# Performance work log

Measured on AMD Instinct MI355X. Metric: run time of the kernel, lower is better.

Reference implementation:

```python
import jax, jax.numpy as jnp
import numpy as np

EPS = 1e-6  # rms_norm_eps
Q_EPS = 1e-5


def activation_quant(x):
    # per-token (last dim) absmax int8 quant
    scale = 127.0 / jnp.clip(jnp.max(jnp.abs(x), axis=-1, keepdims=True), Q_EPS, None)
    return jnp.clip(jnp.round(x * scale), -128, 127) / scale


def weight_quant(w):
    # ternary quant with global mean-absmax scale
    scale = 1.0 / jnp.clip(jnp.mean(jnp.abs(w)), Q_EPS, None)
    return jnp.clip(jnp.round(w * scale), -1, 1) / scale


def bit_linear(x, w):
    # straight-through estimator on both activation and weight quantization
    xq = x + jax.lax.stop_gradient(activation_quant(x) - x)
    wq = w + jax.lax.stop_gradient(weight_quant(w) - w)
    return jnp.einsum('...k,nk->...n', xq, wq)


def rmsnorm(x, w):
    var = jnp.mean(jnp.square(x), axis=-1, keepdims=True)
    return x * jax.lax.rsqrt(var + EPS) * w


def setup_inputs() -> dict:
    key = jax.random.key(0)
    ks = jax.random.split(key, 6)
    B, C, H, D, F, NC = 8, 3, 128, 2048, 8192, 1000
    return {
        'x': jax.random.normal(ks[0], (B, C, H, D), jnp.float32),
        'Wg': jax.random.normal(ks[1], (F, D), jnp.float32) * (D ** -0.5),
        'Wu': jax.random.normal(ks[2], (F, D), jnp.float32) * (D ** -0.5),
        'Wd': jax.random.normal(ks[3], (D, F), jnp.float32) * (F ** -0.5),
        'ln_w': jnp.ones((F,), jnp.float32),
        'cls_W': jax.random.normal(ks[4], (NC, C), jnp.float32) * (C ** -0.5),
        'cls_b': jnp.zeros((NC,), jnp.float32),
    }


def reference(x, Wg, Wu, Wd, ln_w, cls_W, cls_b):
    # BitNet SwiGLU MLP
    h = jax.nn.silu(bit_linear(x, Wg)) * bit_linear(x, Wu)  # [B,3,H,F]
    h = rmsnorm(h, ln_w)
    h = bit_linear(h, Wd)  # [B,3,H,D]
    # classifier: AdaptiveAvgPool2d((1,1)) over last two dims -> [B,3] -> Linear
    pooled = jnp.mean(h, axis=(2, 3))  # [B,3]
    return pooled @ cls_W.T + cls_b  # [B, num_classes]
```

## Files before the change

### kernel.cpp

```cpp
#include <hip/hip_runtime.h>
#include <stdint.h>

#define BB 8
#define CC 3
#define HH 128
#define DD 2048
#define FF 8192
#define NCLS 1000
#define MTOK (BB*CC*HH)
#define NW   (FF*DD)
#define INV_NW (1.0f/16777216.0f)

typedef __attribute__((ext_vector_type(4))) int i32x4;
typedef __attribute__((ext_vector_type(16))) int i32x16;
typedef _Float16 f16x8 __attribute__((ext_vector_type(8)));

#define WS_SUMS    0
#define WS_PART    256
#define WS_POOLED  4096
#define WS_TSUM    16384
#define WS_INVSA   49152
#define WS_XQ      61440
#define WS_WGQ     6352896
#define WS_WUQ     23130112
#define WS_H       39907328
#define WS_NEED    90238976

__device__ __forceinline__ float reduce256(float v, float* red, bool first) {
  for (int off = 32; off > 0; off >>= 1) v += __shfl_xor(v, off);
  if (!first) __syncthreads();
  if ((threadIdx.x & 63) == 0) red[threadIdx.x >> 6] = v;
  __syncthreads();
  return (red[0] + red[1]) + (red[2] + red[3]);
}

__global__ __launch_bounds__(256) void prep_kernel(
    const float* __restrict__ Wg, const float* __restrict__ Wu,
    const float* __restrict__ Wd, const float* __restrict__ x,
    float* __restrict__ part, int8_t* __restrict__ xq,
    float* __restrict__ inv_sa, float* __restrict__ tsum) {
  const int bx = blockIdx.x, t = threadIdx.x;
  if (bx < 768) {
    const int mat = bx >> 8;
    const float* w = (mat == 0) ? Wg : (mat == 1) ? Wu : Wd;
    const float4* w4 = (const float4*)w;
    const unsigned idx = (bx & 255) * 256 + t;
    float s0 = 0.f, s1 = 0.f, s2 = 0.f, s3 = 0.f;
#pragma unroll 4
    for (int it = 0; it < 64; it += 4) {
      float4 a = w4[idx + (size_t)(it + 0) * 65536];
      float4 b = w4[idx + (size_t)(it + 1) * 65536];
      float4 c = w4[idx + (size_t)(it + 2) * 65536];
      float4 d = w4[idx + (size_t)(it + 3) * 65536];
      s0 += fabsf(a.x) + fabsf(a.y) + fabsf(a.z) + fabsf(a.w);
      s1 += fabsf(b.x) + fabsf(b.y) + fabsf(b.z) + fabsf(b.w);
      s2 += fabsf(c.x) + fabsf(c.y) + fabsf(c.z) + fabsf(c.w);
      s3 += fabsf(d.x) + fabsf(d.y) + fabsf(d.z) + fabsf(d.w);
    }
    __shared__ float red[4];
    float total = reduce256((s0 + s1) + (s2 + s3), red, true);
    if (t == 0) part[bx] = total;
  } else if (bx < 3840) {
    const int tok = bx - 768;
    const float* row = x + (size_t)tok * DD;
    float4 v0 = *(const float4*)(row + t * 4);
    float4 v1 = *(const float4*)(row + 1024 + t * 4);
    float mx = fmaxf(fmaxf(fmaxf(fabsf(v0.x), fabsf(v0.y)), fmaxf(fabsf(v0.z), fabsf(v0.w))),
                     fmaxf(fmaxf(fabsf(v1.x), fabsf(v1.y)), fmaxf(fabsf(v1.z), fabsf(v1.w))));
    for (int off = 32; off > 0; off >>= 1) mx = fmaxf(mx, __shfl_xor(mx, off));
    __shared__ float wm[4];
    if ((t & 63) == 0) wm[t >> 6] = mx;
    __syncthreads();
    float m = fmaxf(fmaxf(wm[0], wm[1]), fmaxf(wm[2], wm[3]));
    float mclip = fmaxf(m, 1e-5f);
    float sa = 127.0f / mclip;
    if (t == 0) inv_sa[tok] = mclip * (1.0f / 127.0f);
    float qv[8] = {v0.x, v0.y, v0.z, v0.w, v1.x, v1.y, v1.z, v1.w};
    unsigned p0 = 0, p1 = 0;
#pragma unroll
    for (int j = 0; j < 4; ++j) {
      int qi = (int)fminf(fmaxf(rintf(qv[j] * sa), -128.f), 127.f);
      p0 |= ((unsigned)(qi & 0xff)) << (8 * j);
    }
#pragma unroll
    for (int j = 0; j < 4; ++j) {
      int qi = (int)fminf(fmaxf(rintf(qv[4 + j] * sa), -128.f), 127.f);
      p1 |= ((unsigned)(qi & 0xff)) << (8 * j);
    }
    *(unsigned*)(xq + (size_t)tok * DD + t * 4) = p0;
    *(unsigned*)(xq + (size_t)tok * DD + 1024 + t * 4) = p1;
  } else {
    float4 z = {0.f, 0.f, 0.f, 0.f};
#pragma unroll
    for (int j = 0; j < 8; ++j)
      *(float4*)(tsum + j * 1024 + t * 4) = z;
  }
}

__global__ __launch_bounds__(256) void wquant_kernel(
    const float* __restrict__ Wg, const float* __restrict__ Wu,
    const float* __restrict__ Wd, const float* __restrict__ part,
    float* __restrict__ sums, int8_t* __restrict__ wgq,
    int8_t* __restrict__ wuq, float* __restrict__ tsum) {
  const int bx = blockIdx.x, t = threadIdx.x;
  __shared__ float red[4];
  if (bx < 8192) {
    const int mat = bx >> 12;
    const float* w = mat ? Wu : Wg;
    int8_t* wq = mat ? wuq : wgq;
    const float total = reduce256(part[mat * 256 + t], red, true);
    const float scale = 1.0f / fmaxf(total * INV_NW, 1e-5f);
    const unsigned base = (bx & 4095) * 4096;
    float4 v[4];
#pragma unroll
    for (int j = 0; j < 4; ++j)
      v[j] = *(const float4*)(w + base + j * 1024 + t * 4);
#pragma unroll
    for (int j = 0; j < 4; ++j) {
      float vv[4] = {v[j].x, v[j].y, v[j].z, v[j].w};
      unsigned p = 0;
#pragma unroll
      for (int jj = 0; jj < 4; ++jj) {
        int qi = (int)fminf(fmaxf(rintf(vv[jj] * scale), -1.f), 1.f);
        p |= ((unsigned)(qi & 0xff)) << (8 * jj);
      }
      *(unsigned*)(wq + base + j * 1024 + t * 4) = p;
    }
  } else {
    const int idx = bx - 8192;
    const int slab = idx >> 5, colg = idx & 31;
    const float totalWd = reduce256(part[512 + t], red, true);
    const float scale = 1.0f / fmaxf(totalWd * INV_NW, 1e-5f);
    const int col = colg * 256 + t;
    const float* wp = Wd + (size_t)(slab * 256) * FF + col;
    float acc = 0.f;
#pragma unroll 8
    for (int d = 0; d < 256; ++d)
      acc += fminf(fmaxf(rintf(wp[(size_t)d * FF] * scale), -1.f), 1.f);
    atomicAdd(&tsum[col], acc);
    if (idx == 255) {
      const float tg = reduce256(part[t], red, false);
      const float tu = reduce256(part[256 + t], red, false);
      if (t == 0) { sums[0] = tg; sums[1] = tu; sums[2] = totalWd; }
    }
  }
}

__device__ __forceinline__ void gl_lds16(const void* g, void* l) {
  __builtin_amdgcn_global_load_lds((const __attribute__((address_space(1))) void*)g,
                                   (__attribute__((address_space(3))) void*)l, 16, 0, 0);
}

__global__ __launch_bounds__(256, 4) void gemm_gu_kernel(
    const int8_t* __restrict__ Aq,
    const int8_t* __restrict__ Bgq,
    const int8_t* __restrict__ Buq,
    const float* __restrict__ inv_sa,
    const float* __restrict__ sums,
    _Float16* __restrict__ Hbuf)
{
  __shared__ int8_t ldsA[128 * 128];
  __shared__ int8_t ldsG[64 * 128];
  __shared__ int8_t ldsU[64 * 128];

  const int t = threadIdx.x;
  const int wave = t >> 6, lane = t & 63;
  const int l32 = lane & 31, l5 = lane >> 5;
  const int m0 = blockIdx.x * 128;
  const int n0 = blockIdx.y * 64;
  const int wm = (wave >> 1) * 64, wn = (wave & 1) * 32;

  i32x16 accg[2], accu[2];
#pragma unroll
  for (int i = 0; i < 2; ++i)
#pragma unroll
    for (int r = 0; r < 16; ++r) { accg[i][r] = 0; accu[i][r] = 0; }

  const int srow = lane >> 3;
  const int sp = lane & 7;

  for (int k0 = 0; k0 < DD; k0 += 128) {
    __syncthreads();
#pragma unroll
    for (int j = 0; j < 4; ++j) {
      const int rl = wave * 32 + j * 8 + srow;
      const int cg = sp ^ (rl & 7);
      gl_lds16(Aq + (size_t)(m0 + rl) * DD + k0 + cg * 16,
               ldsA + (wave * 32 + j * 8) * 128);
    }
#pragma unroll
    for (int j = 0; j < 2; ++j) {
      const int rl = wave * 16 + j * 8 + srow;
      const int cg = sp ^ (rl & 7);
      gl_lds16(Bgq + (size_t)(n0 + rl) * DD + k0 + cg * 16,
               ldsG + (wave * 16 + j * 8) * 128);
      gl_lds16(Buq + (size_t)(n0 + rl) * DD + k0 + cg * 16,
               ldsU + (wave * 16 + j * 8) * 128);
    }
    __syncthreads();

#pragma unroll
    for (int ks = 0; ks < 4; ++ks) {
      i32x4 af[2], gfv, ufv;
#pragma unroll
      for (int mt = 0; mt < 2; ++mt) {
        const int row = wm + mt * 32 + l32;
        const int p = (ks * 2 + l5) ^ (row & 7);
        af[mt] = *(const i32x4*)(ldsA + row * 128 + p * 16);
      }
      {
        const int row = wn + l32;
        const int p = (ks * 2 + l5) ^ (row & 7);
        gfv = *(const i32x4*)(ldsG + row * 128 + p * 16);
        ufv = *(const i32x4*)(ldsU + row * 128 + p * 16);
      }
#pragma unroll
      for (int mt = 0; mt < 2; ++mt) {
        accg[mt] = __builtin_amdgcn_mfma_i32_32x32x32_i8(af[mt], gfv, accg[mt], 0, 0, 0);
        accu[mt] = __builtin_amdgcn_mfma_i32_32x32x32_i8(af[mt], ufv, accu[mt], 0, 0, 0);
      }
    }
  }

  const float meanWg = fmaxf(sums[0] * INV_NW, 1e-5f);
  const float meanWu = fmaxf(sums[1] * INV_NW, 1e-5f);
  const int coln = n0 + wn + l32;
#pragma unroll
  for (int mt = 0; mt < 2; ++mt) {
#pragma unroll
    for (int r = 0; r < 16; ++r) {
      const int row = m0 + wm + mt * 32 + (r & 3) + 8 * (r >> 2) + 4 * l5;
      const float isa = inv_sa[row];
      const float g = (float)accg[mt][r] * (isa * meanWg);
      const float u = (float)accu[mt][r] * (isa * meanWu);
      const float sv = g / (1.0f + expf(-g));
      Hbuf[(size_t)row * FF + coln] = (_Float16)(sv * u);
    }
  }
}

__global__ __launch_bounds__(256) void rms_quant_dot_kernel(
    const _Float16* __restrict__ H, const float* __restrict__ lnw,
    const float* __restrict__ tsum, float* __restrict__ pooled) {
  const int tok = blockIdx.x, t = threadIdx.x;
  const _Float16* row = H + (size_t)tok * FF;
  f16x8 hv[4];
  float4 lw[8];
  float ssq = 0.f, mx = 0.f;
#pragma unroll
  for (int i = 0; i < 4; ++i) {
    hv[i] = *(const f16x8*)(row + i * 2048 + t * 8);
    lw[2 * i] = *(const float4*)(lnw + i * 2048 + t * 8);
    lw[2 * i + 1] = *(const float4*)(lnw + i * 2048 + t * 8 + 4);
    const float* lwp = (const float*)&lw[2 * i];
#pragma unroll
    for (int j = 0; j < 8; ++j) {
      float h = (float)hv[i][j];
      ssq += h * h;
      mx = fmaxf(mx, fabsf(h * lwp[j]));
    }
  }
  for (int off = 32; off > 0; off >>= 1) {
    ssq += __shfl_xor(ssq, off);
    mx = fmaxf(mx, __shfl_xor(mx, off));
  }
  __shared__ float rs[4], rm[4], ra[4];
  const int wave = t >> 6, lane = t & 63;
  if (lane == 0) { rs[wave] = ssq; rm[wave] = mx; }
  __syncthreads();
  const float S = (rs[0] + rs[1]) + (rs[2] + rs[3]);
  const float M = fmaxf(fmaxf(rm[0], rm[1]), fmaxf(rm[2], rm[3]));
  const float r = rsqrtf(S * (1.0f / (float)FF) + 1e-6f);
  const float mc = fmaxf(M * r, 1e-5f);
  const float as2 = 127.0f / mc;
  float acc = 0.f;
#pragma unroll
  for (int i = 0; i < 4; ++i) {
    float4 t0 = *(const float4*)(tsum + i * 2048 + t * 8);
    float4 t1 = *(const float4*)(tsum + i * 2048 + t * 8 + 4);
    const float* lwp = (const float*)&lw[2 * i];
    const float* tp0 = (const float*)&t0;
    const float* tp1 = (const float*)&t1;
#pragma unroll
    for (int j = 0; j < 8; ++j) {
      float ts = (j < 4) ? tp0[j] : tp1[j - 4];
      float y = (float)hv[i][j] * lwp[j] * r;
      acc += fminf(fmaxf(rintf(y * as2), -128.f), 127.f) * ts;
    }
  }
  for (int off = 32; off > 0; off >>= 1) acc += __shfl_xor(acc, off);
  if (lane == 0) ra[wave] = acc;
  __syncthreads();
  if (t == 0)
    pooled[tok] = ((ra[0] + ra[1]) + (ra[2] + ra[3])) * (mc * (1.0f / 127.0f));
}

__global__ __launch_bounds__(256) void classifier_kernel(
    const float* __restrict__ pooled, const float* __restrict__ sums,
    const float* __restrict__ clsW, const float* __restrict__ clsb,
    float* __restrict__ out) {
  const int b = blockIdx.x, t = threadIdx.x;
  const float meanWd = fmaxf(sums[2] * INV_NW, 1e-5f);
  const float sc = meanWd * (1.0f / (float)(HH * DD));
  __shared__ float ps[3];
#pragma unroll
  for (int c = 0; c < 3; ++c) {
    float s = 0.f;
    if (t < 64) {
      const float* base = pooled + (b * 3 + c) * 128;
      s = base[t] + base[t + 64];
      for (int off = 32; off > 0; off >>= 1) s += __shfl_xor(s, off);
      if (t == 0) ps[c] = s * sc;
    }
    __syncthreads();
  }
  const float p0 = ps[0], p1 = ps[1], p2 = ps[2];
  for (int n = t; n < NCLS; n += 256)
    out[b * NCLS + n] = clsb[n] + p0 * clsW[n * 3 + 0] + p1 * clsW[n * 3 + 1] + p2 * clsW[n * 3 + 2];
}

extern "C" void kernel_launch(void* const* d_in, const int* in_sizes, int n_in,
                              void* d_out, int out_size, void* d_ws, size_t ws_size,
                              hipStream_t stream) {
  if (n_in < 7 || ws_size < (size_t)WS_NEED) return;
  const float* x = (const float*)d_in[0];
  const float* Wg = (const float*)d_in[1];
  const float* Wu = (const float*)d_in[2];
  const float* Wd = (const float*)d_in[3];
  const float* lnw = (const float*)d_in[4];
  const float* clsW = (const float*)d_in[5];
  const float* clsb = (const float*)d_in[6];
  float* out = (float*)d_out;
  char* ws = (char*)d_ws;
  float* sums = (float*)(ws + WS_SUMS);
  float* part = (float*)(ws + WS_PART);
  float* pooled = (float*)(ws + WS_POOLED);
  float* tsum = (float*)(ws + WS_TSUM);
  float* inv_sa = (float*)(ws + WS_INVSA);
  int8_t* xq = (int8_t*)(ws + WS_XQ);
  int8_t* wgq = (int8_t*)(ws + WS_WGQ);
  int8_t* wuq = (int8_t*)(ws + WS_WUQ);
  _Float16* hbuf = (_Float16*)(ws + WS_H);

  prep_kernel<<<3841, 256, 0, stream>>>(Wg, Wu, Wd, x, part, xq, inv_sa, tsum);
  wquant_kernel<<<8448, 256, 0, stream>>>(Wg, Wu, Wd, part, sums, wgq, wuq, tsum);
  gemm_gu_kernel<<<dim3(24, 128), 256, 0, stream>>>(xq, wgq, wuq, inv_sa, sums, hbuf);
  rms_quant_dot_kernel<<<MTOK, 256, 0, stream>>>(hbuf, lnw, tsum, pooled);
  classifier_kernel<<<BB, 256, 0, stream>>>(pooled, sums, clsW, clsb, out);
  (void)in_sizes; (void)out_size;
}
```

Baseline: 392.4 us.

## Switch gate/up GEMM to 16x16x64 int8 MFMA and rebalance prep/quant grids

The gate/up GEMM now uses 16x16x64 int8 MFMA tiles with a 4x2 accumulator grid per wave in place of 32x32x32 tiles, and lowers the occupancy hint from 4 to 3. The weight abs-sum prep is split into many more small contiguous blocks (6144 partials) and the weight quant kernel gives each block twice as many elements. The Wd column-sum slabs are halved. The aim is higher MFMA throughput, fewer LDS reads per FLOP, and better memory parallelism in the prep stages, at the cost of more accumulator registers and a larger partial-sum reduction.

```diff
diff --git a/kernel.cpp b/kernel.cpp
--- a/kernel.cpp
+++ b/kernel.cpp
@@ -12,19 +12,18 @@
 #define INV_NW (1.0f/16777216.0f)
 
 typedef __attribute__((ext_vector_type(4))) int i32x4;
-typedef __attribute__((ext_vector_type(16))) int i32x16;
 typedef _Float16 f16x8 __attribute__((ext_vector_type(8)));
 
 #define WS_SUMS    0
 #define WS_PART    256
-#define WS_POOLED  4096
-#define WS_TSUM    16384
-#define WS_INVSA   49152
-#define WS_XQ      61440
-#define WS_WGQ     6352896
-#define WS_WUQ     23130112
-#define WS_H       39907328
-#define WS_NEED    90238976
+#define WS_POOLED  24832
+#define WS_TSUM    37120
+#define WS_INVSA   69888
+#define WS_XQ      82176
+#define WS_WGQ     6373632
+#define WS_WUQ     23150848
+#define WS_H       39928064
+#define WS_NEED    90259712
 
 __device__ __forceinline__ float reduce256(float v, float* red, bool first) {
   for (int off = 32; off > 0; off >>= 1) v += __shfl_xor(v, off);
@@ -40,28 +39,22 @@
     float* __restrict__ part, int8_t* __restrict__ xq,
     float* __restrict__ inv_sa, float* __restrict__ tsum) {
   const int bx = blockIdx.x, t = threadIdx.x;
-  if (bx < 768) {
-    const int mat = bx >> 8;
+  if (bx < 6144) {
+    const int mat = bx >> 11;
     const float* w = (mat == 0) ? Wg : (mat == 1) ? Wu : Wd;
-    const float4* w4 = (const float4*)w;
-    const unsigned idx = (bx & 255) * 256 + t;
-    float s0 = 0.f, s1 = 0.f, s2 = 0.f, s3 = 0.f;
-#pragma unroll 4
-    for (int it = 0; it < 64; it += 4) {
-      float4 a = w4[idx + (size_t)(it + 0) * 65536];
-      float4 b = w4[idx + (size_t)(it + 1) * 65536];
-      float4 c = w4[idx + (size_t)(it + 2) * 65536];
-      float4 d = w4[idx + (size_t)(it + 3) * 65536];
-      s0 += fabsf(a.x) + fabsf(a.y) + fabsf(a.z) + fabsf(a.w);
-      s1 += fabsf(b.x) + fabsf(b.y) + fabsf(b.z) + fabsf(b.w);
-      s2 += fabsf(c.x) + fabsf(c.y) + fabsf(c.z) + fabsf(c.w);
-      s3 += fabsf(d.x) + fabsf(d.y) + fabsf(d.z) + fabsf(d.w);
-    }
+    const float4* w4 = (const float4*)w + (size_t)(bx & 2047) * 2048;
+    float4 v[8];
+#pragma unroll
+    for (int j = 0; j < 8; ++j) v[j] = w4[j * 256 + t];
+    float s = 0.f;
+#pragma unroll
+    for (int j = 0; j < 8; ++j)
+      s += fabsf(v[j].x) + fabsf(v[j].y) + fabsf(v[j].z) + fabsf(v[j].w);
     __shared__ float red[4];
-    float total = reduce256((s0 + s1) + (s2 + s3), red, true);
+    float total = reduce256(s, red, true);
     if (t == 0) part[bx] = total;
-  } else if (bx < 3840) {
-    const int tok = bx - 768;
+  } else if (bx < 9216) {
+    const int tok = bx - 6144;
     const float* row = x + (size_t)tok * DD;
     float4 v0 = *(const float4*)(row + t * 4);
     float4 v1 = *(const float4*)(row + 1024 + t * 4);
@@ -104,19 +97,22 @@
     int8_t* __restrict__ wuq, float* __restrict__ tsum) {
   const int bx = blockIdx.x, t = threadIdx.x;
   __shared__ float red[4];
-  if (bx < 8192) {
-    const int mat = bx >> 12;
+  if (bx < 4096) {
+    const int mat = bx >> 11;
     const float* w = mat ? Wu : Wg;
     int8_t* wq = mat ? wuq : wgq;
-    const float total = reduce256(part[mat * 256 + t], red, true);
+    float ps = 0.f;
+#pragma unroll
+    for (int j = 0; j < 8; ++j) ps += part[mat * 2048 + j * 256 + t];
+    const float total = reduce256(ps, red, true);
     const float scale = 1.0f / fmaxf(total * INV_NW, 1e-5f);
-    const unsigned base = (bx & 4095) * 4096;
-    float4 v[4];
-#pragma unroll
-    for (int j = 0; j < 4; ++j)
+    const size_t base = (size_t)(bx & 2047) * 8192;
+    float4 v[8];
+#pragma unroll
+    for (int j = 0; j < 8; ++j)
       v[j] = *(const float4*)(w + base + j * 1024 + t * 4);
 #pragma unroll
-    for (int j = 0; j < 4; ++j) {
+    for (int j = 0; j < 8; ++j) {
       float vv[4] = {v[j].x, v[j].y, v[j].z, v[j].w};
       unsigned p = 0;
 #pragma unroll
@@ -127,20 +123,26 @@
       *(unsigned*)(wq + base + j * 1024 + t * 4) = p;
     }
   } else {
-    const int idx = bx - 8192;
+    const int idx = bx - 4096;
     const int slab = idx >> 5, colg = idx & 31;
-    const float totalWd = reduce256(part[512 + t], red, true);
+    float ps = 0.f;
+#pragma unroll
+    for (int j = 0; j < 8; ++j) ps += part[4096 + j * 256 + t];
+    const float totalWd = reduce256(ps, red, true);
     const float scale = 1.0f / fmaxf(totalWd * INV_NW, 1e-5f);
     const int col = colg * 256 + t;
-    const float* wp = Wd + (size_t)(slab * 256) * FF + col;
+    const float* wp = Wd + (size_t)(slab * 128) * FF + col;
     float acc = 0.f;
 #pragma unroll 8
-    for (int d = 0; d < 256; ++d)
+    for (int d = 0; d < 128; ++d)
       acc += fminf(fmaxf(rintf(wp[(size_t)d * FF] * scale), -1.f), 1.f);
     atomicAdd(&tsum[col], acc);
-    if (idx == 255) {
-      const float tg = reduce256(part[t], red, false);
-      const float tu = reduce256(part[256 + t], red, false);
+    if (idx == 511) {
+      float pg = 0.f, pu = 0.f;
+#pragma unroll
+      for (int j = 0; j < 8; ++j) { pg += part[j * 256 + t]; pu += part[2048 + j * 256 + t]; }
+      const float tg = reduce256(pg, red, false);
+      const float tu = reduce256(pu, red, false);
       if (t == 0) { sums[0] = tg; sums[1] = tu; sums[2] = totalWd; }
     }
   }
@@ -151,7 +153,7 @@
                                    (__attribute__((address_space(3))) void*)l, 16, 0, 0);
 }
 
-__global__ __launch_bounds__(256, 4) void gemm_gu_kernel(
+__global__ __launch_bounds__(256, 3) void gemm_gu_kernel(
     const int8_t* __restrict__ Aq,
     const int8_t* __restrict__ Bgq,
     const int8_t* __restrict__ Buq,
@@ -165,16 +167,16 @@
 
   const int t = threadIdx.x;
   const int wave = t >> 6, lane = t & 63;
-  const int l32 = lane & 31, l5 = lane >> 5;
+  const int q = lane >> 4, ln = lane & 15;
   const int m0 = blockIdx.x * 128;
   const int n0 = blockIdx.y * 64;
   const int wm = (wave >> 1) * 64, wn = (wave & 1) * 32;
 
-  i32x16 accg[2], accu[2];
-#pragma unroll
-  for (int i = 0; i < 2; ++i)
-#pragma unroll
-    for (int r = 0; r < 16; ++r) { accg[i][r] = 0; accu[i][r] = 0; }
+  i32x4 accg[4][2], accu[4][2];
+#pragma unroll
+  for (int i = 0; i < 4; ++i)
+#pragma unroll
+    for (int j = 0; j < 2; ++j) { accg[i][j] = i32x4{0,0,0,0}; accu[i][j] = i32x4{0,0,0,0}; }
 
   const int srow = lane >> 3;
   const int sp = lane & 7;
@@ -200,41 +202,48 @@
     __syncthreads();
 
 #pragma unroll
-    for (int ks = 0; ks < 4; ++ks) {
-      i32x4 af[2], gfv, ufv;
-#pragma unroll
-      for (int mt = 0; mt < 2; ++mt) {
-        const int row = wm + mt * 32 + l32;
-        const int p = (ks * 2 + l5) ^ (row & 7);
+    for (int s = 0; s < 2; ++s) {
+      i32x4 af[4], gf[2], uf[2];
+#pragma unroll
+      for (int mt = 0; mt < 4; ++mt) {
+        const int row = wm + mt * 16 + ln;
+        const int p = (s * 4 + q) ^ (row & 7);
         af[mt] = *(const i32x4*)(ldsA + row * 128 + p * 16);
       }
-      {
-        const int row = wn + l32;
-        const int p = (ks * 2 + l5) ^ (row & 7);
-        gfv = *(const i32x4*)(ldsG + row * 128 + p * 16);
-        ufv = *(const i32x4*)(ldsU + row * 128 + p * 16);
+#pragma unroll
+      for (int nt = 0; nt < 2; ++nt) {
+        const int row = wn + nt * 16 + ln;
+        const int p = (s * 4 + q) ^ (row & 7);
+        gf[nt] = *(const i32x4*)(ldsG + row * 128 + p * 16);
+        uf[nt] = *(const i32x4*)(ldsU + row * 128 + p * 16);
       }
 #pragma unroll
-      for (int mt = 0; mt < 2; ++mt) {
-        accg[mt] = __builtin_amdgcn_mfma_i32_32x32x32_i8(af[mt], gfv, accg[mt], 0, 0, 0);
-        accu[mt] = __builtin_amdgcn_mfma_i32_32x32x32_i8(af[mt], ufv, accu[mt], 0, 0, 0);
-      }
+      for (int mt = 0; mt < 4; ++mt)
+#pragma unroll
+        for (int nt = 0; nt < 2; ++nt) {
+          accg[mt][nt] = __builtin_amdgcn_mfma_i32_16x16x64_i8(af[mt], gf[nt], accg[mt][nt], 0, 0, 0);
+          accu[mt][nt] = __builtin_amdgcn_mfma_i32_16x16x64_i8(af[mt], uf[nt], accu[mt][nt], 0, 0, 0);
+        }
     }
   }
 
   const float meanWg = fmaxf(sums[0] * INV_NW, 1e-5f);
   const float meanWu = fmaxf(sums[1] * INV_NW, 1e-5f);
-  const int coln = n0 + wn + l32;
-#pragma unroll
-  for (int mt = 0; mt < 2; ++mt) {
-#pragma unroll
-    for (int r = 0; r < 16; ++r) {
-      const int row = m0 + wm + mt * 32 + (r & 3) + 8 * (r >> 2) + 4 * l5;
+#pragma unroll
+  for (int mt = 0; mt < 4; ++mt) {
+#pragma unroll
+    for (int r = 0; r < 4; ++r) {
+      const int row = m0 + wm + mt * 16 + q * 4 + r;
       const float isa = inv_sa[row];
-      const float g = (float)accg[mt][r] * (isa * meanWg);
-      const float u = (float)accu[mt][r] * (isa * meanWu);
-      const float sv = g / (1.0f + expf(-g));
-      Hbuf[(size_t)row * FF + coln] = (_Float16)(sv * u);
+      const float sg = isa * meanWg, su = isa * meanWu;
+      _Float16* hrow = Hbuf + (size_t)row * FF + n0 + wn;
+#pragma unroll
+      for (int nt = 0; nt < 2; ++nt) {
+        const float g = (float)accg[mt][nt][r] * sg;
+        const float u = (float)accu[mt][nt][r] * su;
+        const float sv = g / (1.0f + expf(-g));
+        hrow[nt * 16 + ln] = (_Float16)(sv * u);
+      }
     }
   }
 }
@@ -342,8 +351,8 @@
   int8_t* wuq = (int8_t*)(ws + WS_WUQ);
   _Float16* hbuf = (_Float16*)(ws + WS_H);
 
-  prep_kernel<<<3841, 256, 0, stream>>>(Wg, Wu, Wd, x, part, xq, inv_sa, tsum);
-  wquant_kernel<<<8448, 256, 0, stream>>>(Wg, Wu, Wd, part, sums, wgq, wuq, tsum);
+  prep_kernel<<<9217, 256, 0, stream>>>(Wg, Wu, Wd, x, part, xq, inv_sa, tsum);
+  wquant_kernel<<<4608, 256, 0, stream>>>(Wg, Wu, Wd, part, sums, wgq, wuq, tsum);
   gemm_gu_kernel<<<dim3(24, 128), 256, 0, stream>>>(xq, wgq, wuq, inv_sa, sums, hbuf);
   rms_quant_dot_kernel<<<MTOK, 256, 0, stream>>>(hbuf, lnw, tsum, pooled);
   classifier_kernel<<<BB, 256, 0, stream>>>(pooled, sums, clsW, clsb, out);
```

New measurement: 374.8 us. 1.05x faster.
